# Optimization experiments

Hardware: AMD Instinct MI355X
Metric: run time of the kernel (lower is better)

Reference implementation:

```python
import jax, jax.numpy as jnp
import numpy as np

D_MODEL = 1024
N_HEADS = 16
HEAD_DIM = D_MODEL // N_HEADS


def setup_inputs() -> dict:
    key = jax.random.key(0)
    ks = jax.random.split(key, 5)
    B, T = 2, 2048
    x = jax.random.normal(ks[0], (B, T, D_MODEL), dtype=jnp.float32)
    s = 1.0 / np.sqrt(D_MODEL)
    qkv_w = jax.random.uniform(ks[1], (3 * D_MODEL, D_MODEL), jnp.float32, -s, s)
    qkv_b = jax.random.uniform(ks[2], (3 * D_MODEL,), jnp.float32, -s, s)
    out_w = jax.random.uniform(ks[3], (D_MODEL, D_MODEL), jnp.float32, -s, s)
    out_b = jax.random.uniform(ks[4], (D_MODEL,), jnp.float32, -s, s)
    return {"x": x, "qkv_w": qkv_w, "qkv_b": qkv_b, "out_w": out_w, "out_b": out_b}


def reference(x, qkv_w, qkv_b, out_w, out_b):
    B, T, _ = x.shape
    # qkv projection: [B,T,3*D]
    qkv = x @ qkv_w.T + qkv_b
    qkv = qkv.reshape(B, T, 3, N_HEADS, HEAD_DIM)
    qkv = jnp.transpose(qkv, (2, 0, 3, 1, 4))  # [3,B,H,T,Hd]
    q, k, v = qkv[0], qkv[1], qkv[2]
    scale = 1.0 / np.sqrt(HEAD_DIM)
    scores = jnp.einsum("bhqd,bhkd->bhqk", q, k) * scale  # [B,H,T,T]
    causal = jnp.tril(jnp.ones((T, T), dtype=bool))
    scores = jnp.where(causal, scores, -jnp.inf)
    weights = jax.nn.softmax(scores, axis=-1)
    # dropout in eval mode (identity)
    out = jnp.einsum("bhqk,bhkd->bhqd", weights, v)  # [B,H,T,Hd]
    out = jnp.transpose(out, (0, 2, 1, 3)).reshape(B, T, D_MODEL)
    return out @ out_w.T + out_b
```

## Files before the change

kernel.cpp:

```cpp
#include <hip/hip_runtime.h>
#include <hip/hip_bf16.h>


typedef __bf16 bf16;
typedef bf16 bf16x8 __attribute__((ext_vector_type(8)));
typedef bf16 bf16x4 __attribute__((ext_vector_type(4)));
typedef float f32x4 __attribute__((ext_vector_type(4)));

#define MFMA16(a, b, c) __builtin_amdgcn_mfma_f32_16x16x32_bf16((a), (b), (c), 0, 0, 0)

static constexpr int D_MODEL = 1024;
static constexpr int NH = 16;
static constexpr int HD = 64;
static constexpr int SEQ = 2048;
static constexpr int NB = 2;
static constexpr float QSCALE = 0.125f * 1.44269504088896340736f;

__device__ __forceinline__ bf16x8 cvt8(const float* p) {
    float4 u0 = *(const float4*)p;
    float4 u1 = *(const float4*)(p + 4);
    bf16x8 v = { (bf16)u0.x, (bf16)u0.y, (bf16)u0.z, (bf16)u0.w,
                 (bf16)u1.x, (bf16)u1.y, (bf16)u1.z, (bf16)u1.w };
    return v;
}

__device__ __forceinline__ void async16(const bf16* g, bf16* l) {
    __builtin_amdgcn_global_load_lds(
        (const __attribute__((address_space(1))) void*)g,
        (__attribute__((address_space(3))) void*)l, 16, 0, 0);
}

__global__ __launch_bounds__(256)
void k_cast(const float* __restrict__ in, bf16* __restrict__ out, int n8)
{
    int i = blockIdx.x * 256 + threadIdx.x;
    if (i < n8) *(bf16x8*)&out[(size_t)i * 8] = cvt8(&in[(size_t)i * 8]);
}

__global__ __launch_bounds__(256)
void k_qkv(const bf16* __restrict__ x, const bf16* __restrict__ w,
           const float* __restrict__ bias,
           bf16* __restrict__ Qb, bf16* __restrict__ Kb, bf16* __restrict__ VbT)
{
    __shared__ bf16 As[128 * 32];
    __shared__ bf16 Ws[128 * 32];

    const int tid  = threadIdx.x;
    const int wv   = tid >> 6;
    const int lane = tid & 63;
    const int lr   = lane & 15;
    const int lk   = lane >> 4;
    const int wm   = wv >> 1, wn = wv & 1;
    const int m0   = blockIdx.x * 128;
    const int n0   = blockIdx.y * 128;

    const int sRow = tid >> 2;
    const int sCol = (tid & 3) * 8;
    const int sOff = sRow * 32 + sCol;

    f32x4 acc[4][4] = {};

    for (int kt = 0; kt < 1024; kt += 32) {
        __syncthreads();
        async16(&x[(size_t)(m0 + sRow     ) * 1024 + kt + sCol], &As[sOff]);
        async16(&x[(size_t)(m0 + 64 + sRow) * 1024 + kt + sCol], &As[64 * 32 + sOff]);
        async16(&w[(size_t)(n0 + sRow     ) * 1024 + kt + sCol], &Ws[sOff]);
        async16(&w[(size_t)(n0 + 64 + sRow) * 1024 + kt + sCol], &Ws[64 * 32 + sOff]);
        __syncthreads();

        bf16x8 a[4], b[4];
        #pragma unroll
        for (int i = 0; i < 4; i++) {
            a[i] = *(const bf16x8*)&As[(wm * 64 + i * 16 + lr) * 32 + lk * 8];
            b[i] = *(const bf16x8*)&Ws[(wn * 64 + i * 16 + lr) * 32 + lk * 8];
        }
        #pragma unroll
        for (int i = 0; i < 4; i++)
            #pragma unroll
            for (int j = 0; j < 4; j++)
                acc[i][j] = MFMA16(a[i], b[j], acc[i][j]);
    }

    #pragma unroll
    for (int i = 0; i < 4; i++) {
        #pragma unroll
        for (int j = 0; j < 4; j++) {
            const int gm0 = m0 + wm * 64 + i * 16 + lk * 4;
            const int gn  = n0 + wn * 64 + j * 16 + lr;
            const int sel = gn >> 10;
            const int rem = gn & 1023;
            const int h   = rem >> 6;
            const int hd  = rem & 63;
            const int bb  = gm0 >> 11;
            const int t0  = gm0 & 2047;
            if (sel == 2) {
                bf16x4 p;
                #pragma unroll
                for (int r = 0; r < 4; r++) p[r] = (bf16)(acc[i][j][r] + bias[gn]);
                *(bf16x4*)&VbT[((size_t)(bb * NH + h) * HD + hd) * SEQ + t0] = p;
            } else {
                #pragma unroll
                for (int r = 0; r < 4; r++) {
                    float v = acc[i][j][r] + bias[gn];
                    size_t idx = ((size_t)(bb * NH + h) * SEQ + t0 + r) * HD + hd;
                    if (sel == 0) Qb[idx] = (bf16)(v * QSCALE);
                    else          Kb[idx] = (bf16)v;
                }
            }
        }
    }
}

__global__ __launch_bounds__(256)
void k_attn(const bf16* __restrict__ Qb, const bf16* __restrict__ Kb,
            const bf16* __restrict__ VbT, bf16* __restrict__ AO)
{
    __shared__ bf16 Ks[64][72];
    __shared__ bf16 Vt[64][72];
    __shared__ bf16 Ps[64][72];

    const int tid  = threadIdx.x;
    const int wv   = tid >> 6;
    const int lane = tid & 63;
    const int lr   = lane & 15;
    const int lk   = lane >> 4;
    const int bh   = blockIdx.y;
    const int qt   = ((bh >> 3) & 1) ? (31 - (int)blockIdx.x) : (int)blockIdx.x;

    const bf16* Qp  = Qb  + (size_t)bh * SEQ * HD;
    const bf16* Kp  = Kb  + (size_t)bh * SEQ * HD;
    const bf16* Vtp = VbT + (size_t)bh * HD * SEQ;

    const int qg = qt * 64 + wv * 16 + lr;

    bf16x8 qf[2];
    qf[0] = *(const bf16x8*)&Qp[(size_t)qg * HD +      lk * 8];
    qf[1] = *(const bf16x8*)&Qp[(size_t)qg * HD + 32 + lk * 8];

    f32x4 ot[4] = {};
    float lsum = 0.f;

    const int r0 = tid >> 3;
    const int c0 = (tid & 7) * 8;

    for (int kt = 0; kt <= qt; kt++) {
        const int k0 = kt * 64;
        __syncthreads();
        *(bf16x8*)&Ks[r0     ][c0] = *(const bf16x8*)&Kp[(size_t)(k0 + r0     ) * HD + c0];
        *(bf16x8*)&Ks[r0 + 32][c0] = *(const bf16x8*)&Kp[(size_t)(k0 + r0 + 32) * HD + c0];
        *(bf16x8*)&Vt[r0     ][c0] = *(const bf16x8*)&Vtp[(size_t)(r0     ) * SEQ + k0 + c0];
        *(bf16x8*)&Vt[r0 + 32][c0] = *(const bf16x8*)&Vtp[(size_t)(r0 + 32) * SEQ + k0 + c0];
        __syncthreads();

        f32x4 s[4] = {};
        #pragma unroll
        for (int j = 0; j < 4; j++) {
            #pragma unroll
            for (int c = 0; c < 2; c++) {
                bf16x8 ka = *(const bf16x8*)&Ks[j * 16 + lr][c * 32 + lk * 8];
                s[j] = MFMA16(ka, qf[c], s[j]);
            }
        }

        const bool diag = (kt == qt);
        #pragma unroll
        for (int j = 0; j < 4; j++) {
            const int keyb = k0 + j * 16 + lk * 4;
            f32x4 p;
            #pragma unroll
            for (int r = 0; r < 4; r++) {
                float e = __builtin_amdgcn_exp2f(s[j][r]);
                if (diag) e = (keyb + r > qg) ? 0.f : e;
                p[r] = e;
            }
            s[j] = p;
            lsum += (p[0] + p[1]) + (p[2] + p[3]);
        }

        #pragma unroll
        for (int j = 0; j < 4; j++) {
            bf16x4 p4 = { (bf16)s[j][0], (bf16)s[j][1], (bf16)s[j][2], (bf16)s[j][3] };
            *(bf16x4*)&Ps[wv * 16 + lr][j * 16 + lk * 4] = p4;
        }

        #pragma unroll
        for (int c = 0; c < 2; c++) {
            bf16x8 pb = *(const bf16x8*)&Ps[wv * 16 + lr][c * 32 + lk * 8];
            #pragma unroll
            for (int jh = 0; jh < 4; jh++) {
                bf16x8 va = *(const bf16x8*)&Vt[jh * 16 + lr][c * 32 + lk * 8];
                ot[jh] = MFMA16(va, pb, ot[jh]);
            }
        }
    }

    lsum += __shfl_xor(lsum, 16);
    lsum += __shfl_xor(lsum, 32);

    const float inv = 1.0f / lsum;
    const int b_ = bh >> 4, h_ = bh & 15;
    const size_t base = ((size_t)(b_ * SEQ + qg)) * D_MODEL + h_ * HD;
    #pragma unroll
    for (int jh = 0; jh < 4; jh++) {
        bf16x4 o4 = { (bf16)(ot[jh][0] * inv), (bf16)(ot[jh][1] * inv),
                      (bf16)(ot[jh][2] * inv), (bf16)(ot[jh][3] * inv) };
        *(bf16x4*)&AO[base + jh * 16 + lk * 4] = o4;
    }
}

__global__ __launch_bounds__(256)
void k_oproj(const bf16* __restrict__ a_, const bf16* __restrict__ w,
             const float* __restrict__ bias, float* __restrict__ out)
{
    __shared__ bf16 As[128 * 32];
    __shared__ bf16 Ws[64 * 32];

    const int tid  = threadIdx.x;
    const int wv   = tid >> 6;
    const int lane = tid & 63;
    const int lr   = lane & 15;
    const int lk   = lane >> 4;
    const int wm   = wv >> 1, wn = wv & 1;
    const int m0   = blockIdx.x * 128;
    const int n0   = blockIdx.y * 64;

    const int sRow = tid >> 2;
    const int sCol = (tid & 3) * 8;
    const int sOff = sRow * 32 + sCol;

    f32x4 acc[4][2] = {};

    for (int kt = 0; kt < 1024; kt += 32) {
        __syncthreads();
        async16(&a_[(size_t)(m0 + sRow     ) * 1024 + kt + sCol], &As[sOff]);
        async16(&a_[(size_t)(m0 + 64 + sRow) * 1024 + kt + sCol], &As[64 * 32 + sOff]);
        async16(&w [(size_t)(n0 + sRow     ) * 1024 + kt + sCol], &Ws[sOff]);
        __syncthreads();

        bf16x8 a[4], b[2];
        #pragma unroll
        for (int i = 0; i < 4; i++)
            a[i] = *(const bf16x8*)&As[(wm * 64 + i * 16 + lr) * 32 + lk * 8];
        #pragma unroll
        for (int j = 0; j < 2; j++)
            b[j] = *(const bf16x8*)&Ws[(wn * 32 + j * 16 + lr) * 32 + lk * 8];
        #pragma unroll
        for (int i = 0; i < 4; i++)
            #pragma unroll
            for (int j = 0; j < 2; j++)
                acc[i][j] = MFMA16(a[i], b[j], acc[i][j]);
    }

    #pragma unroll
    for (int i = 0; i < 4; i++) {
        #pragma unroll
        for (int j = 0; j < 2; j++) {
            #pragma unroll
            for (int r = 0; r < 4; r++) {
                int gm = m0 + wm * 64 + i * 16 + lk * 4 + r;
                int gn = n0 + wn * 32 + j * 16 + lr;
                out[(size_t)gm * 1024 + gn] = acc[i][j][r] + bias[gn];
            }
        }
    }
}

extern "C" void kernel_launch(void* const* d_in, const int* in_sizes, int n_in,
                              void* d_out, int out_size, void* d_ws, size_t ws_size,
                              hipStream_t stream)
{
    const float* x     = (const float*)d_in[0];
    const float* qkv_w = (const float*)d_in[1];
    const float* qkv_b = (const float*)d_in[2];
    const float* out_w = (const float*)d_in[3];
    const float* out_b = (const float*)d_in[4];
    float* out = (float*)d_out;

    const size_t SZ = (size_t)NB * NH * SEQ * HD;
    bf16* Qb  = (bf16*)d_ws;
    bf16* Kb  = Qb + SZ;
    bf16* VbT = Kb + SZ;
    bf16* AO  = VbT + SZ;
    bf16* xb  = AO + SZ;
    bf16* wqb = xb + SZ;
    bf16* wob = wqb + (size_t)3 * D_MODEL * D_MODEL;

    hipLaunchKernelGGL(k_cast, dim3(2048), dim3(256), 0, stream, x,     xb,  524288);
    hipLaunchKernelGGL(k_cast, dim3(1536), dim3(256), 0, stream, qkv_w, wqb, 393216);
    hipLaunchKernelGGL(k_cast, dim3(512),  dim3(256), 0, stream, out_w, wob, 131072);

    hipLaunchKernelGGL(k_qkv, dim3(32, 24), dim3(256), 0, stream,
                       xb, wqb, qkv_b, Qb, Kb, VbT);
    hipLaunchKernelGGL(k_attn, dim3(32, 32), dim3(256), 0, stream,
                       Qb, Kb, VbT, AO);
    hipLaunchKernelGGL(k_oproj, dim3(32, 16), dim3(256), 0, stream,
                       AO, wob, out_b, out);
}
```

Measured before the change: 203.0 us.

## Double-buffer K/V tiles with async global-to-LDS loads and XOR-swizzled layout

The attention kernel now stages the next K and V tiles into a second LDS buffer with async global-to-LDS copies while the current tile is computed, using vmcnt waits and raw barriers in place of two __syncthreads per iteration. The padded LDS arrays become unpadded tiles with an XOR swizzle on 16-byte chunks, applied to the K, V and P buffers, so bank conflicts stay avoided without padding. The intent is to hide global load latency behind MFMA work. LDS use grows because K and V are double-buffered, and correctness depends on async16 and the hand-written waitcnt counts being right.

New measurement: 176.2 us. 13.2% less time.

```diff
diff --git a/kernel.cpp b/kernel.cpp
--- a/kernel.cpp
+++ b/kernel.cpp
@@ -115,9 +115,9 @@
 void k_attn(const bf16* __restrict__ Qb, const bf16* __restrict__ Kb,
             const bf16* __restrict__ VbT, bf16* __restrict__ AO)
 {
-    __shared__ bf16 Ks[64][72];
-    __shared__ bf16 Vt[64][72];
-    __shared__ bf16 Ps[64][72];
+    __shared__ bf16 Ks[2][64 * 64];
+    __shared__ bf16 Vt[2][64 * 64];
+    __shared__ bf16 Ps[64 * 64];
 
     const int tid  = threadIdx.x;
     const int wv   = tid >> 6;
@@ -140,58 +140,78 @@
     f32x4 ot[4] = {};
     float lsum = 0.f;
 
-    const int r0 = tid >> 3;
-    const int c0 = (tid & 7) * 8;
+    const int srow   = tid >> 3;
+    const int sgcol  = ((tid & 7) ^ (srow & 7)) * 8;
+    const int sldse  = tid * 8;
+    const int swz    = lr & 7;
+
+    auto stage = [&](int buf, int k0) {
+        async16(&Kp [(size_t)(k0 + srow     ) * HD  + sgcol], &Ks[buf][       sldse]);
+        async16(&Kp [(size_t)(k0 + 32 + srow) * HD  + sgcol], &Ks[buf][2048 + sldse]);
+        async16(&Vtp[(size_t)(srow          ) * SEQ + k0 + sgcol], &Vt[buf][       sldse]);
+        async16(&Vtp[(size_t)(32 + srow     ) * SEQ + k0 + sgcol], &Vt[buf][2048 + sldse]);
+    };
+
+    stage(0, 0);
 
     for (int kt = 0; kt <= qt; kt++) {
+        const int p = kt & 1;
+        if (kt < qt) {
+            stage(p ^ 1, (kt + 1) * 64);
+            asm volatile("s_waitcnt vmcnt(4)" ::: "memory");
+        } else {
+            asm volatile("s_waitcnt vmcnt(0)" ::: "memory");
+        }
+        __builtin_amdgcn_s_barrier();
+
+        f32x4 s[4] = {};
+        #pragma unroll
+        for (int j = 0; j < 4; j++) {
+            #pragma unroll
+            for (int c = 0; c < 2; c++) {
+                bf16x8 ka = *(const bf16x8*)
+                    &Ks[p][(j * 16 + lr) * 64 + (((4 * c + lk) ^ swz) << 3)];
+                s[j] = MFMA16(ka, qf[c], s[j]);
+            }
+        }
+
         const int k0 = kt * 64;
-        __syncthreads();
-        *(bf16x8*)&Ks[r0     ][c0] = *(const bf16x8*)&Kp[(size_t)(k0 + r0     ) * HD + c0];
-        *(bf16x8*)&Ks[r0 + 32][c0] = *(const bf16x8*)&Kp[(size_t)(k0 + r0 + 32) * HD + c0];
-        *(bf16x8*)&Vt[r0     ][c0] = *(const bf16x8*)&Vtp[(size_t)(r0     ) * SEQ + k0 + c0];
-        *(bf16x8*)&Vt[r0 + 32][c0] = *(const bf16x8*)&Vtp[(size_t)(r0 + 32) * SEQ + k0 + c0];
-        __syncthreads();
-
-        f32x4 s[4] = {};
-        #pragma unroll
-        for (int j = 0; j < 4; j++) {
-            #pragma unroll
-            for (int c = 0; c < 2; c++) {
-                bf16x8 ka = *(const bf16x8*)&Ks[j * 16 + lr][c * 32 + lk * 8];
-                s[j] = MFMA16(ka, qf[c], s[j]);
-            }
-        }
-
         const bool diag = (kt == qt);
         #pragma unroll
         for (int j = 0; j < 4; j++) {
             const int keyb = k0 + j * 16 + lk * 4;
-            f32x4 p;
+            f32x4 pv;
             #pragma unroll
             for (int r = 0; r < 4; r++) {
                 float e = __builtin_amdgcn_exp2f(s[j][r]);
                 if (diag) e = (keyb + r > qg) ? 0.f : e;
-                p[r] = e;
-            }
-            s[j] = p;
-            lsum += (p[0] + p[1]) + (p[2] + p[3]);
+                pv[r] = e;
+            }
+            s[j] = pv;
+            lsum += (pv[0] + pv[1]) + (pv[2] + pv[3]);
         }
 
         #pragma unroll
         for (int j = 0; j < 4; j++) {
             bf16x4 p4 = { (bf16)s[j][0], (bf16)s[j][1], (bf16)s[j][2], (bf16)s[j][3] };
-            *(bf16x4*)&Ps[wv * 16 + lr][j * 16 + lk * 4] = p4;
+            *(bf16x4*)&Ps[(wv * 16 + lr) * 64 +
+                          (((2 * j + (lk >> 1)) ^ swz) << 3) + ((lk & 1) << 2)] = p4;
         }
 
         #pragma unroll
         for (int c = 0; c < 2; c++) {
-            bf16x8 pb = *(const bf16x8*)&Ps[wv * 16 + lr][c * 32 + lk * 8];
+            bf16x8 pb = *(const bf16x8*)
+                &Ps[(wv * 16 + lr) * 64 + (((4 * c + lk) ^ swz) << 3)];
             #pragma unroll
             for (int jh = 0; jh < 4; jh++) {
-                bf16x8 va = *(const bf16x8*)&Vt[jh * 16 + lr][c * 32 + lk * 8];
+                bf16x8 va = *(const bf16x8*)
+                    &Vt[p][(jh * 16 + lr) * 64 + (((4 * c + lk) ^ swz) << 3)];
                 ot[jh] = MFMA16(va, pb, ot[jh]);
             }
         }
+
+        asm volatile("" ::: "memory");
+        __builtin_amdgcn_s_barrier();
     }
 
     lsum += __shfl_xor(lsum, 16);
```
